# Kernel tuning notes

Measured on AMD Instinct MI355X. Metric: run time of the kernel, lower is better.

Reference implementation:

```python
import jax, jax.numpy as jnp
import numpy as np

B, L, D, N, NBLK = 16, 2048, 256, 64, 6  # 6 S4D layers: blocks 1,2,3,5 + 2 inner layers of FS4Ddeq


def setup_inputs() -> dict:
    key = jax.random.key(0)
    ks = jax.random.split(key, 12)
    x = jax.random.normal(ks[0], (B, L), dtype=jnp.float32)
    W_emb = jax.random.normal(ks[1], (1, D), dtype=jnp.float32) * 0.1
    b_emb = jnp.zeros((D,), jnp.float32)
    # S4D parameters, stacked over the 6 layers
    log_dt = jax.random.uniform(ks[2], (NBLK, D), minval=float(np.log(1e-3)), maxval=float(np.log(1e-1)), dtype=jnp.float32)
    logAre = jnp.full((NBLK, D, N), float(np.log(0.5)), jnp.float32)
    Aim = jnp.broadcast_to(jnp.pi * jnp.arange(N, dtype=jnp.float32), (NBLK, D, N)) * jnp.ones((NBLK, D, N), jnp.float32)
    Cre = jax.random.normal(ks[3], (NBLK, D, N), dtype=jnp.float32) * (0.5 ** 0.5)
    Cim = jax.random.normal(ks[4], (NBLK, D, N), dtype=jnp.float32) * (0.5 ** 0.5)
    Dskip = jax.random.normal(ks[5], (NBLK, D), dtype=jnp.float32)
    Wout = jax.random.normal(ks[6], (NBLK, D, D), dtype=jnp.float32) / np.sqrt(D)
    bout = jnp.zeros((NBLK, D), jnp.float32)
    gamma = jnp.ones((NBLK, D), jnp.float32)
    beta = jnp.zeros((NBLK, D), jnp.float32)
    # feedforward of the FS4Ddeq block (feed_size=[B,L,emb_dim], feed_act='relu')
    feed_W1 = jax.random.normal(ks[7], (D, D), dtype=jnp.float32) / np.sqrt(D)
    feed_b1 = jnp.zeros((D,), jnp.float32)
    feed_W2 = jax.random.normal(ks[8], (D, D), dtype=jnp.float32) / np.sqrt(D)
    feed_b2 = jnp.zeros((D,), jnp.float32)
    fc_W = jax.random.normal(ks[9], (D, 2), dtype=jnp.float32) / np.sqrt(D)
    fc_b = jnp.zeros((2,), jnp.float32)
    return dict(x=x, W_emb=W_emb, b_emb=b_emb, log_dt=log_dt, logAre=logAre, Aim=Aim,
                Cre=Cre, Cim=Cim, Dskip=Dskip, Wout=Wout, bout=bout, gamma=gamma, beta=beta,
                feed_W1=feed_W1, feed_b1=feed_b1, feed_W2=feed_W2, feed_b2=feed_b2,
                fc_W=fc_W, fc_b=fc_b)


def _s4d_block(h, log_dt, logAre, Aim, Cre, Cim, Dskip, Wout, bout, gamma, beta):
    """Pre-norm (BN eval-mode) -> diagonal SSM (ZOH, FFT conv) -> GELU -> Linear -> residual."""
    _, Lh, _ = h.shape
    z = gamma * h + beta  # BatchNorm in eval mode with identity running stats
    dt = jnp.exp(log_dt)[:, None]                      # [D,1]
    A = -jnp.exp(logAre) + 1j * Aim                    # [D,N] diagonal state matrix
    dtA = dt * A                                       # [D,N]
    C = (Cre + 1j * Cim) * (jnp.exp(dtA) - 1.0) / A    # ZOH-discretized C*B
    # Vandermonde kernel K[d,l] = 2*Re sum_n C[d,n] * exp(dtA[d,n])^l
    vand = jnp.exp(dtA[:, :, None] * jnp.arange(Lh, dtype=jnp.float32))  # [D,N,L]
    K = 2.0 * jnp.einsum('dn,dnl->dl', C, vand).real   # [D,L]
    u = jnp.transpose(z, (0, 2, 1))                    # [B,D,L]
    kf = jnp.fft.rfft(K, n=2 * Lh)
    uf = jnp.fft.rfft(u, n=2 * Lh)
    y = jnp.fft.irfft(uf * kf, n=2 * Lh)[..., :Lh]     # causal conv
    y = y + Dskip[:, None] * u                         # feedthrough D
    y = jax.nn.gelu(jnp.transpose(y, (0, 2, 1)))       # [B,L,D]
    y = jnp.einsum('bld,de->ble', y, Wout) + bout      # output projection
    return y + h                                       # skip connection


def reference(x, W_emb, b_emb, log_dt, logAre, Aim, Cre, Cim, Dskip, Wout, bout,
              gamma, beta, feed_W1, feed_b1, feed_W2, feed_b2, fc_W, fc_b):
    h = x[..., None] @ W_emb + b_emb  # nn.Linear(1, emb_dim): [B,L,D]
    # layers 1,2,3,5: S4D blocks (dropout is identity in eval mode)
    for i in range(4):
        h = _s4d_block(h, log_dt[i], logAre[i], Aim[i], Cre[i], Cim[i],
                       Dskip[i], Wout[i], bout[i], gamma[i], beta[i])
    # layer4: FS4Ddeq_model with layers=2 inner S4D blocks + relu feed net + final relu + skip
    r = h
    for i in (4, 5):
        h = _s4d_block(h, log_dt[i], logAre[i], Aim[i], Cre[i], Cim[i],
                       Dskip[i], Wout[i], bout[i], gamma[i], beta[i])
    h = jax.nn.relu(h @ feed_W1 + feed_b1) @ feed_W2 + feed_b2
    h = jax.nn.relu(h + r)
    mean_y = jnp.mean(h, axis=1)       # [B,D]
    logits = mean_y @ fc_W + fc_b      # [B,2]
    return logits
```

## Files before the change

### kernel.cpp

```cpp
#include <hip/hip_runtime.h>
#include <hip/hip_fp16.h>
#include <math.h>

#define B_ 16
#define L_ 2048
#define D_ 256
#define N_ 64
#define NBLK_ 6
#define LC_ 128
#define NC_ 16

typedef _Float16 half8 __attribute__((ext_vector_type(8)));
typedef float f32x4 __attribute__((ext_vector_type(4)));

__device__ __forceinline__ unsigned short f2h(float f) {
  _Float16 h = (_Float16)f;
  return *(unsigned short*)&h;
}
__device__ __forceinline__ float h2f(unsigned short u) {
  _Float16 h = *(_Float16*)&u;
  return (float)h;
}

__global__ void precompute_kernel(const float* __restrict__ log_dt,
                                  const float* __restrict__ logAre,
                                  const float* __restrict__ Aim,
                                  const float* __restrict__ Cre,
                                  const float* __restrict__ Cim,
                                  float* __restrict__ wbuf,
                                  float* __restrict__ c2buf,
                                  float* __restrict__ wlbuf) {
  int idx = blockIdx.x * blockDim.x + threadIdx.x;
  if (idx >= NBLK_ * D_ * N_) return;
  int blk = idx >> 14;
  int rem = idx & 16383;
  int d = rem >> 6;
  int n = rem & 63;
  float dt   = expf(log_dt[blk * D_ + d]);
  float are  = -expf(logAre[idx]);
  float aim  = Aim[idx];
  float dtar = dt * are, dtai = dt * aim;
  float er = expf(dtar);
  float wr = er * cosf(dtai);
  float wi = er * sinf(dtai);
  float inv = 1.0f / (are * are + aim * aim);
  float wm1r = wr - 1.0f;
  float br = (wm1r * are + wi * aim) * inv;
  float bi = (wi * are - wm1r * aim) * inv;
  float crv = Cre[idx], civ = Cim[idx];
  float c2r = 2.0f * (crv * br - civ * bi);
  float c2i = 2.0f * (crv * bi + civ * br);
  float eL = expf((float)LC_ * dtar);
  float angL = (float)LC_ * dtai;
  float* wb = wbuf + (size_t)((blk << 8) + d) * 128;
  wb[n] = wr; wb[64 + n] = wi;
  float* cb = c2buf + (size_t)((blk << 8) + d) * 128;
  cb[n] = c2r; cb[64 + n] = c2i;
  wlbuf[2 * idx] = eL * cosf(angL); wlbuf[2 * idx + 1] = eL * sinf(angL);
}

__global__ __launch_bounds__(256) void build_all(
    const float* __restrict__ WB, const float* __restrict__ C2B,
    const float* __restrict__ WLB,
    const float* __restrict__ gamma_, const float* __restrict__ beta_,
    const float* __restrict__ dskip,
    unsigned short* __restrict__ TnA, unsigned short* __restrict__ EnA,
    unsigned short* __restrict__ FnA, float* __restrict__ PbetaA,
    float* __restrict__ SbetaA) {
  __shared__ float Pr[128][65];
  __shared__ float Pi_[128][65];
  __shared__ float wc[256];
  __shared__ float Kt[128];
  int bid = blockIdx.x;
  int blk = bid >> 8, d = bid & 255;
  int t = threadIdx.x;
  if (t < 128) wc[t] = WB[(size_t)((blk << 8) + d) * 128 + t];
  else         wc[t] = C2B[(size_t)((blk << 8) + d) * 128 + (t - 128)];
  __syncthreads();
  int n = t & 63, tj = t >> 6;
  float wr = wc[n], wi = wc[64 + n];
  float gd = gamma_[blk * D_ + d], bd = beta_[blk * D_ + d], dsk = dskip[blk * D_ + d];
  {
    int j0 = tj << 5;
    float pr = 1.f, pi = 0.f, br = wr, bi = wi;
    int e = j0;
    while (e) {
      if (e & 1) { float tt = pr * br - pi * bi; pi = pr * bi + pi * br; pr = tt; }
      float t2 = br * br - bi * bi; bi = 2.f * br * bi; br = t2;
      e >>= 1;
    }
#pragma unroll 4
    for (int k = 0; k < 32; ++k) {
      Pr[j0 + k][n] = pr; Pi_[j0 + k][n] = pi;
      float tt = pr * wr - pi * wi; pi = pr * wi + pi * wr; pr = tt;
    }
  }
  __syncthreads();
  if (t < 128) {
    float kc = 0.f;
    for (int nn = 0; nn < 64; ++nn)
      kc += wc[128 + nn] * Pr[t][nn] - wc[192 + nn] * Pi_[t][nn];
    Kt[t] = kc + (t == 0 ? dsk : 0.f);
  }
  size_t mbase = (size_t)(blk * 256 + d) * 16384;
#pragma unroll
  for (int r8 = 0; r8 < 8; ++r8) {
    int task = t + (r8 << 8);
    int j = task >> 4, g = task & 15;
    int half = g >> 3, n0 = (g & 7) << 3;
    unsigned short v[8];
#pragma unroll
    for (int i = 0; i < 8; ++i) {
      int nn = n0 + i;
      float pr = Pr[j][nn], pi = Pi_[j][nn];
      float wwr = wc[nn], wwi = wc[64 + nn];
      float qr = pr * wwr - pi * wwi, qi = pr * wwi + pi * wwr;
      float cr = wc[128 + nn], ci = wc[192 + nn];
      v[i] = f2h(half == 0 ? (cr * qr - ci * qi) : (cr * qi + ci * qr));
    }
    *(uint4*)(EnA + mbase + (size_t)j * 128 + (half << 6) + n0) = *(uint4*)v;
  }
#pragma unroll
  for (int r8 = 0; r8 < 8; ++r8) {
    int task = t + (r8 << 8);
    int n2 = task >> 4, tb = task & 15;
    int half = n2 >> 6, nn = n2 & 63;
    int tau0 = tb << 3;
    unsigned short v[8];
#pragma unroll
    for (int i = 0; i < 8; ++i) {
      int j = 127 - (tau0 + i);
      v[i] = f2h(half == 0 ? (gd * Pr[j][nn]) : (-gd * Pi_[j][nn]));
    }
    *(uint4*)(FnA + mbase + (size_t)n2 * 128 + tau0) = *(uint4*)v;
  }
  __syncthreads();
  if (t < 128) {
    float ps = 0.f;
    for (int t2 = 0; t2 <= t; ++t2) ps += Kt[t2];
    PbetaA[((size_t)blk * 256 + d) * 128 + t] = bd * ps;
  }
  if (t >= 128 && t < 192) {
    int nn = t - 128;
    const float* wlp = WLB + (((size_t)((blk << 8) + d)) * 64 + nn) * 2;
    float wlr = wlp[0], wli = wlp[1];
    float wwr = wc[nn], wwi = wc[64 + nn];
    float nr = wlr - 1.f, ni = wli, dr2 = wwr - 1.f, di = wwi;
    float iv = 1.f / (dr2 * dr2 + di * di);
    SbetaA[((size_t)blk * 256 + d) * 128 + nn]      = bd * ((nr * dr2 + ni * di) * iv);
    SbetaA[((size_t)blk * 256 + d) * 128 + 64 + nn] = bd * (-((ni * dr2 - nr * di) * iv));
  }
  int chunk = t & 15, rg = t >> 4;
#pragma unroll
  for (int it = 0; it < 8; ++it) {
    int trow = (it << 4) + rg;
    int tau0 = chunk << 3;
    unsigned short v[8];
#pragma unroll
    for (int i = 0; i < 8; ++i) {
      int tau = tau0 + i;
      v[i] = (tau <= trow) ? f2h(gd * Kt[trow - tau]) : (unsigned short)0;
    }
    *(uint4*)(TnA + mbase + (size_t)trow * 128 + tau0) = *(uint4*)v;
  }
}

__global__ void embed_kernel(const float* __restrict__ x, const float* __restrict__ wemb,
                             const float* __restrict__ bemb, unsigned short* __restrict__ H) {
  int tid = blockIdx.x * blockDim.x + threadIdx.x;
  if (tid >= B_ * L_ * D_) return;
  int d = tid & (D_ - 1);
  int lg = tid >> 8;
  H[tid] = f2h(fmaf(x[lg], wemb[d], bemb[d]));
}

__global__ __launch_bounds__(256) void trans_h_ut(const unsigned short* __restrict__ H,
                                                  unsigned short* __restrict__ UT) {
  __shared__ __align__(16) unsigned short lds[64][136];
  int bi = blockIdx.x;
  int bc = bi >> 2, dq = bi & 3;
  int b = bc >> 4, ch = bc & 15;
  int tid = threadIdx.x;
  const unsigned short* src = H + ((size_t)(b * L_ + ch * 128)) * D_ + dq * 64;
  int tau0 = tid >> 4;
  int dl = (tid & 15) << 2;
  for (int tt = 0; tt < 128; tt += 16) {
    ushort4 v = *(const ushort4*)(src + (size_t)(tt + tau0) * D_ + dl);
    lds[dl + 0][tt + tau0] = v.x;
    lds[dl + 1][tt + tau0] = v.y;
    lds[dl + 2][tt + tau0] = v.z;
    lds[dl + 3][tt + tau0] = v.w;
  }
  __syncthreads();
  int r = tid >> 2, seg = (tid & 3) << 5;
  unsigned short* dst = UT + ((size_t)((dq * 64 + r) * 256 + bc)) * 128 + seg;
  const unsigned short* srow = &lds[r][seg];
  *(uint4*)(dst + 0)  = *(const uint4*)(srow + 0);
  *(uint4*)(dst + 8)  = *(const uint4*)(srow + 8);
  *(uint4*)(dst + 16) = *(const uint4*)(srow + 16);
  *(uint4*)(dst + 24) = *(const uint4*)(srow + 24);
}

__global__ __launch_bounds__(256) void scan_fused(
    const unsigned short* __restrict__ UT, const unsigned short* __restrict__ FnA,
    const unsigned short* __restrict__ TnA, const unsigned short* __restrict__ EnA,
    const float* __restrict__ SbetaA, const float* __restrict__ PbetaA,
    const float* __restrict__ WLB, unsigned short* __restrict__ GT, int blk) {
  __shared__ __align__(16) unsigned short SLl[256 * 136];
  __shared__ __align__(16) unsigned short AsB[128 * 40];
  __shared__ __align__(16) unsigned short BsB[128 * 40];
  _Float16* As = (_Float16*)AsB;
  _Float16* Bs = (_Float16*)BsB;
  int d = blockIdx.x;
  int tid = threadIdx.x, lane = tid & 63, w = tid >> 6;
  int wm = (w & 1) << 6, wn = (w >> 1) << 6;
  int r = tid & 127, sg = (tid >> 7) << 4;
  int cn = lane & 15, rq = lane >> 4;
  int ko = (lane >> 4) << 3;
  const unsigned short* Au = UT + (size_t)d * 256 * 128;
  const unsigned short* Bf = FnA + (size_t)(blk * 256 + d) * 16384;
  const unsigned short* Bt = TnA + (size_t)(blk * 256 + d) * 16384;
  const unsigned short* Be = EnA + (size_t)(blk * 256 + d) * 16384;
  size_t pb = ((size_t)blk * 256 + d) * 128;

  for (int mh = 0; mh < 2; ++mh) {
    const unsigned short* Ab = Au + (size_t)(mh << 7) * 128;
    f32x4 acc[4][4];
#pragma unroll
    for (int a = 0; a < 4; ++a)
#pragma unroll
      for (int b2 = 0; b2 < 4; ++b2) acc[a][b2] = (f32x4){0.f, 0.f, 0.f, 0.f};
    uint4 a0 = *(const uint4*)(Ab + (size_t)r * 128 + sg);
    uint4 a1 = *(const uint4*)(Ab + (size_t)r * 128 + sg + 8);
    uint4 b0 = *(const uint4*)(Bf + (size_t)r * 128 + sg);
    uint4 b1 = *(const uint4*)(Bf + (size_t)r * 128 + sg + 8);
    for (int kc = 0; kc < 128; kc += 32) {
      __syncthreads();
      *(uint4*)&As[r * 40 + sg] = a0; *(uint4*)&As[r * 40 + sg + 8] = a1;
      *(uint4*)&Bs[r * 40 + sg] = b0; *(uint4*)&Bs[r * 40 + sg + 8] = b1;
      __syncthreads();
      if (kc < 96) {
        a0 = *(const uint4*)(Ab + (size_t)r * 128 + kc + 32 + sg);
        a1 = *(const uint4*)(Ab + (size_t)r * 128 + kc + 32 + sg + 8);
        b0 = *(const uint4*)(Bf + (size_t)r * 128 + kc + 32 + sg);
        b1 = *(const uint4*)(Bf + (size_t)r * 128 + kc + 32 + sg + 8);
      }
      half8 af[4], bf4[4];
#pragma unroll
      for (int mf = 0; mf < 4; ++mf) af[mf] = *(const half8*)&As[(wm + (mf << 4) + cn) * 40 + ko];
#pragma unroll
      for (int nf = 0; nf < 4; ++nf) bf4[nf] = *(const half8*)&Bs[(wn + (nf << 4) + cn) * 40 + ko];
#pragma unroll
      for (int mf = 0; mf < 4; ++mf)
#pragma unroll
        for (int nf = 0; nf < 4; ++nf)
          acc[mf][nf] = __builtin_amdgcn_mfma_f32_16x16x32_f16(af[mf], bf4[nf], acc[mf][nf], 0, 0, 0);
    }
#pragma unroll
    for (int nf = 0; nf < 4; ++nf) {
      int nl = wn + (nf << 4) + cn;
      float sb = SbetaA[pb + nl];
#pragma unroll
      for (int mf = 0; mf < 4; ++mf)
#pragma unroll
        for (int rr = 0; rr < 4; ++rr) {
          int row = (mh << 7) + wm + (mf << 4) + (rq << 2) + rr;
          SLl[row * 136 + nl] = f2h(acc[mf][nf][rr] + sb);
        }
    }
  }
  __syncthreads();

  for (int task = tid; task < 1024; task += 256) {
    int b = task >> 6, n = task & 63;
    const float* wlp = WLB + (((size_t)((blk << 8) + d)) * 64 + n) * 2;
    float wlr = wlp[0], wli = wlp[1];
    float Sr = 0.f, Sj = 0.f;
    for (int c = 0; c < NC_; ++c) {
      int row = (b << 4) + c;
      float tr2 = h2f(SLl[row * 136 + n]);
      float tj  = h2f(SLl[row * 136 + 64 + n]);
      SLl[row * 136 + n]      = f2h(Sr);
      SLl[row * 136 + 64 + n] = f2h(Sj);
      float nSr = fmaf(wlr, Sr, fmaf(wli, Sj, tr2));
      Sj = fmaf(-wli, Sr, fmaf(wlr, Sj, tj));
      Sr = nSr;
    }
  }
  __syncthreads();

  for (int mh = 0; mh < 2; ++mh) {
    const unsigned short* Ab = Au + (size_t)(mh << 7) * 128;
    const _Float16* SA = (const _Float16*)SLl + (size_t)(mh << 7) * 136;
    f32x4 acc[4][4];
#pragma unroll
    for (int a = 0; a < 4; ++a)
#pragma unroll
      for (int b2 = 0; b2 < 4; ++b2) acc[a][b2] = (f32x4){0.f, 0.f, 0.f, 0.f};
    uint4 a0 = *(const uint4*)(Ab + (size_t)r * 128 + sg);
    uint4 a1 = *(const uint4*)(Ab + (size_t)r * 128 + sg + 8);
    uint4 b0 = *(const uint4*)(Bt + (size_t)r * 128 + sg);
    uint4 b1 = *(const uint4*)(Bt + (size_t)r * 128 + sg + 8);
    for (int kb = 0; kb < 8; ++kb) {
      __syncthreads();
      if (kb < 4) { *(uint4*)&As[r * 40 + sg] = a0; *(uint4*)&As[r * 40 + sg + 8] = a1; }
      *(uint4*)&Bs[r * 40 + sg] = b0; *(uint4*)&Bs[r * 40 + sg + 8] = b1;
      __syncthreads();
      if (kb < 3) {
        int kc = (kb + 1) << 5;
        a0 = *(const uint4*)(Ab + (size_t)r * 128 + kc + sg);
        a1 = *(const uint4*)(Ab + (size_t)r * 128 + kc + sg + 8);
        b0 = *(const uint4*)(Bt + (size_t)r * 128 + kc + sg);
        b1 = *(const uint4*)(Bt + (size_t)r * 128 + kc + sg + 8);
      } else if (kb < 7) {
        int kc = (kb - 3) << 5;
        b0 = *(const uint4*)(Be + (size_t)r * 128 + kc + sg);
        b1 = *(const uint4*)(Be + (size_t)r * 128 + kc + sg + 8);
      }
      half8 af[4], bf4[4];
      if (kb < 4) {
#pragma unroll
        for (int mf = 0; mf < 4; ++mf) af[mf] = *(const half8*)&As[(wm + (mf << 4) + cn) * 40 + ko];
      } else {
        int kof = ((kb - 4) << 5) + ko;
#pragma unroll
        for (int mf = 0; mf < 4; ++mf) af[mf] = *(const half8*)&SA[(wm + (mf << 4) + cn) * 136 + kof];
      }
#pragma unroll
      for (int nf = 0; nf < 4; ++nf) bf4[nf] = *(const half8*)&Bs[(wn + (nf << 4) + cn) * 40 + ko];
#pragma unroll
      for (int mf = 0; mf < 4; ++mf)
#pragma unroll
        for (int nf = 0; nf < 4; ++nf)
          acc[mf][nf] = __builtin_amdgcn_mfma_f32_16x16x32_f16(af[mf], bf4[nf], acc[mf][nf], 0, 0, 0);
    }
    __syncthreads();
    unsigned short* epi = SLl + (size_t)(mh << 7) * 136;
#pragma unroll
    for (int nf = 0; nf < 4; ++nf) {
      int nl = wn + (nf << 4) + cn;
      float pb2 = PbetaA[pb + nl];
#pragma unroll
      for (int mf = 0; mf < 4; ++mf)
#pragma unroll
        for (int rr = 0; rr < 4; ++rr) {
          int ml = wm + (mf << 4) + (rq << 2) + rr;
          float xx = acc[mf][nf][rr] + pb2;
          float x3 = xx * xx * xx;
          float inner = 0.7978845608028654f * fmaf(0.044715f, x3, xx);
          float e = __expf(-2.f * fabsf(inner));
          float th = (1.f - e) / (1.f + e);
          th = copysignf(th, inner);
          epi[ml * 136 + nl] = f2h(0.5f * xx * (1.f + th));
        }
    }
    __syncthreads();
    int mr = tid >> 1, hf = (tid & 1) << 6;
    size_t gb = ((size_t)d * 256 + (mh << 7) + mr) * 128 + hf;
#pragma unroll
    for (int k = 0; k < 8; ++k)
      *(uint4*)(GT + gb + k * 8) = *(const uint4*)&epi[mr * 136 + hf + k * 8];
  }
}

__global__ void wprep_kernel(const float* __restrict__ Wout, const float* __restrict__ fW1,
                             const float* __restrict__ fW2, unsigned short* __restrict__ WT) {
  __shared__ float tile[64][65];
  int wv = blockIdx.x >> 4;
  int tk = (blockIdx.x >> 2) & 3;
  int tn = blockIdx.x & 3;
  const float* src = (wv < 6) ? (Wout + (size_t)wv * 65536) : (wv == 6 ? fW1 : fW2);
  int r = threadIdx.x >> 4;
  int c = (threadIdx.x & 15) << 2;
  for (int rr = 0; rr < 64; rr += 16) {
    float4 v = *(const float4*)(src + (size_t)(tk * 64 + r + rr) * 256 + tn * 64 + c);
    tile[r + rr][c] = v.x; tile[r + rr][c + 1] = v.y;
    tile[r + rr][c + 2] = v.z; tile[r + rr][c + 3] = v.w;
  }
  __syncthreads();
  for (int rr = 0; rr < 64; rr += 16) {
    int n = r + rr;
    ushort4 o;
    o.x = f2h(tile[c + 0][n]); o.y = f2h(tile[c + 1][n]);
    o.z = f2h(tile[c + 2][n]); o.w = f2h(tile[c + 3][n]);
    *(ushort4*)(WT + (size_t)wv * 65536 + (size_t)(tn * 64 + n) * 256 + tk * 64 + c) = o;
  }
}

__global__ __launch_bounds__(256, 2) void gemm_gt(const unsigned short* __restrict__ GT,
    const unsigned short* __restrict__ Wt, const float* __restrict__ bias,
    const unsigned short* __restrict__ res, unsigned short* __restrict__ hout,
    unsigned short* __restrict__ ut_next) {
  __shared__ __align__(16) unsigned short smem[18432];
  unsigned short* As = smem;
  unsigned short* Bs = smem + 9216;
  int tid = threadIdx.x;
  int bid = blockIdx.x;
  int bc = bid & 255;
  int m0 = bc * 128, n0 = (bid >> 8) << 7;
  int lane = tid & 63, w = tid >> 6;
  int wm = (w & 1) << 6, wn = (w >> 1) << 6;
  int rb = tid >> 3, cb = (tid & 7) << 3;
  int dr = tid >> 2, sg = (tid & 3) << 5;
  f32x4 acc[4][4];
#pragma unroll
  for (int mf = 0; mf < 4; ++mf)
#pragma unroll
    for (int nf = 0; nf < 4; ++nf) acc[mf][nf] = (f32x4){0.f, 0.f, 0.f, 0.f};

  uint4 gv[4], bv[4];
  {
    const uint4* grow = (const uint4*)(GT + ((size_t)(dr * 256 + bc)) * 128 + sg);
    gv[0] = grow[0]; gv[1] = grow[1]; gv[2] = grow[2]; gv[3] = grow[3];
#pragma unroll
    for (int rr = 0; rr < 4; ++rr)
      bv[rr] = *(const uint4*)(Wt + (size_t)(n0 + rb + rr * 32) * 256 + cb);
  }
  for (int kb = 0; kb < 4; ++kb) {
    __syncthreads();
    const unsigned short* pv = (const unsigned short*)gv;
#pragma unroll
    for (int i = 0; i < 32; ++i) As[(sg + i) * 72 + dr] = pv[i];
#pragma unroll
    for (int rr = 0; rr < 4; ++rr) *(uint4*)&Bs[(rb + rr * 32) * 72 + cb] = bv[rr];
    __syncthreads();
    if (kb < 3) {
      int k0 = (kb + 1) << 6;
      const uint4* grow = (const uint4*)(GT + ((size_t)((k0 + dr) * 256 + bc)) * 128 + sg);
      gv[0] = grow[0]; gv[1] = grow[1]; gv[2] = grow[2]; gv[3] = grow[3];
#pragma unroll
      for (int rr = 0; rr < 4; ++rr)
        bv[rr] = *(const uint4*)(Wt + (size_t)(n0 + rb + rr * 32) * 256 + k0 + cb);
    }
#pragma unroll
    for (int kw = 0; kw < 2; ++kw) {
      int ko = (kw << 5) + ((lane >> 4) << 3);
      half8 af[4], bfr[4];
#pragma unroll
      for (int mf = 0; mf < 4; ++mf)
        af[mf] = *(const half8*)&As[(wm + (mf << 4) + (lane & 15)) * 72 + ko];
#pragma unroll
      for (int nf = 0; nf < 4; ++nf)
        bfr[nf] = *(const half8*)&Bs[(wn + (nf << 4) + (lane & 15)) * 72 + ko];
#pragma unroll
      for (int mf = 0; mf < 4; ++mf)
#pragma unroll
        for (int nf = 0; nf < 4; ++nf)
          acc[mf][nf] = __builtin_amdgcn_mfma_f32_16x16x32_f16(af[mf], bfr[nf], acc[mf][nf], 0, 0, 0);
    }
  }
  int cn = lane & 15, rq = lane >> 4;
  __syncthreads();
  unsigned short* epi = smem;
#pragma unroll
  for (int nf = 0; nf < 4; ++nf) {
    int nl = wn + (nf << 4) + cn;
    float bv2 = bias[n0 + nl];
#pragma unroll
    for (int mf = 0; mf < 4; ++mf)
#pragma unroll
      for (int r = 0; r < 4; ++r) {
        int ml = wm + (mf << 4) + (rq << 2) + r;
        float v = acc[mf][nf][r] + bv2 + h2f(res[(size_t)(m0 + ml) * 256 + n0 + nl]);
        epi[ml * 136 + nl] = f2h(v);
      }
  }
  __syncthreads();
  {
    int mr = tid >> 1, hf = (tid & 1) << 6;
    unsigned short* dst = hout + (size_t)(m0 + mr) * 256 + n0 + hf;
    const unsigned short* srow = epi + mr * 136 + hf;
#pragma unroll
    for (int k = 0; k < 8; ++k) *(uint4*)(dst + k * 8) = *(const uint4*)(srow + k * 8);
  }
  if (ut_next) {
    int nl = tid >> 1, h2 = (tid & 1) << 6;
    unsigned short* dst = ut_next + ((size_t)(n0 + nl) * 256 + bc) * 128 + h2;
#pragma unroll
    for (int k = 0; k < 8; ++k) {
      unsigned short v8[8];
#pragma unroll
      for (int e = 0; e < 8; ++e) v8[e] = epi[(h2 + k * 8 + e) * 136 + nl];
      *(uint4*)(dst + k * 8) = *(uint4*)v8;
    }
  }
}

__global__ __launch_bounds__(256, 2) void gemm_ffn(const unsigned short* __restrict__ A,
    const unsigned short* __restrict__ Wt, const float* __restrict__ bias,
    const unsigned short* __restrict__ res, unsigned short* __restrict__ outp) {
  __shared__ __align__(16) unsigned short smem[18432];
  unsigned short* As = smem;
  unsigned short* Bs = smem + 9216;
  int tid = threadIdx.x;
  int bid = blockIdx.x;
  int m0 = (bid & 255) << 7, n0 = (bid >> 8) << 7;
  int lane = tid & 63, w = tid >> 6;
  int wm = (w & 1) << 6, wn = (w >> 1) << 6;
  int r0 = tid >> 3;
  int c0 = (tid & 7) << 3;
  f32x4 acc[4][4];
#pragma unroll
  for (int mf = 0; mf < 4; ++mf)
#pragma unroll
    for (int nf = 0; nf < 4; ++nf) acc[mf][nf] = (f32x4){0.f, 0.f, 0.f, 0.f};

  uint4 av[4], bv[4];
#pragma unroll
  for (int rr = 0; rr < 4; ++rr) {
    int r = r0 + rr * 32;
    av[rr] = *(const uint4*)(A + (size_t)(m0 + r) * 256 + c0);
    bv[rr] = *(const uint4*)(Wt + (size_t)(n0 + r) * 256 + c0);
  }
  for (int kb = 0; kb < 4; ++kb) {
    __syncthreads();
#pragma unroll
    for (int rr = 0; rr < 4; ++rr) {
      int r = r0 + rr * 32;
      *(uint4*)&As[r * 72 + c0] = av[rr];
      *(uint4*)&Bs[r * 72 + c0] = bv[rr];
    }
    __syncthreads();
    if (kb < 3) {
      int k0 = (kb + 1) << 6;
#pragma unroll
      for (int rr = 0; rr < 4; ++rr) {
        int r = r0 + rr * 32;
        av[rr] = *(const uint4*)(A + (size_t)(m0 + r) * 256 + k0 + c0);
        bv[rr] = *(const uint4*)(Wt + (size_t)(n0 + r) * 256 + k0 + c0);
      }
    }
#pragma unroll
    for (int kw = 0; kw < 2; ++kw) {
      int ko = (kw << 5) + ((lane >> 4) << 3);
      half8 af[4], bfr[4];
#pragma unroll
      for (int mf = 0; mf < 4; ++mf)
        af[mf] = *(const half8*)&As[(wm + (mf << 4) + (lane & 15)) * 72 + ko];
#pragma unroll
      for (int nf = 0; nf < 4; ++nf)
        bfr[nf] = *(const half8*)&Bs[(wn + (nf << 4) + (lane & 15)) * 72 + ko];
#pragma unroll
      for (int mf = 0; mf < 4; ++mf)
#pragma unroll
        for (int nf = 0; nf < 4; ++nf)
          acc[mf][nf] = __builtin_amdgcn_mfma_f32_16x16x32_f16(af[mf], bfr[nf], acc[mf][nf], 0, 0, 0);
    }
  }
  int cn = lane & 15, rq = lane >> 4;
  __syncthreads();
  unsigned short* epi = smem;
#pragma unroll
  for (int nf = 0; nf < 4; ++nf) {
    int nl = wn + (nf << 4) + cn;
#pragma unroll
    for (int mf = 0; mf < 4; ++mf)
#pragma unroll
      for (int r = 0; r < 4; ++r) {
        int ml = wm + (mf << 4) + (rq << 2) + r;
        epi[ml * 136 + nl] = f2h(acc[mf][nf][r]);
      }
  }
  __syncthreads();
  int mr = tid >> 1, hf = (tid & 1) << 6;
  unsigned short* dst = outp + (size_t)(m0 + mr) * 256 + n0 + hf;
#pragma unroll
  for (int k = 0; k < 8; ++k) {
    uint4 c = *(const uint4*)&epi[mr * 136 + hf + k * 8];
    uint4 rv = (uint4){0, 0, 0, 0};
    if (res) rv = *(const uint4*)(res + (size_t)(m0 + mr) * 256 + n0 + hf + k * 8);
    const unsigned short* cp = (const unsigned short*)&c;
    const unsigned short* rp = (const unsigned short*)&rv;
    unsigned short o8[8];
#pragma unroll
    for (int e = 0; e < 8; ++e) {
      float v = h2f(cp[e]) + bias[n0 + hf + k * 8 + e];
      if (res) v += h2f(rp[e]);
      o8[e] = f2h(fmaxf(v, 0.f));
    }
    *(uint4*)(dst + k * 8) = *(uint4*)o8;
  }
}

__global__ void head1_kernel(const unsigned short* __restrict__ H, float* __restrict__ part) {
  int b = blockIdx.x, ls = blockIdx.y, d = threadIdx.x;
  const unsigned short* p = H + ((size_t)(b * L_ + ls * 128)) * D_ + d;
  float sum = 0.f;
  for (int l = 0; l < 128; ++l) sum += h2f(p[(size_t)l * D_]);
  part[(b * 16 + ls) * D_ + d] = sum;
}

__global__ void head2_kernel(const float* __restrict__ part, const float* __restrict__ fcW,
                             const float* __restrict__ fcb, float* __restrict__ out) {
  int b = blockIdx.x, d = threadIdx.x;
  float sum = 0.f;
  for (int i = 0; i < 16; ++i) sum += part[(b * 16 + i) * D_ + d];
  __shared__ float meanv[D_];
  meanv[d] = sum * (1.0f / (float)L_);
  __syncthreads();
  if (d < 2) {
    float accv = fcb[d];
    for (int k = 0; k < D_; ++k) accv = fmaf(meanv[k], fcW[k * 2 + d], accv);
    out[b * 2 + d] = accv;
  }
}

extern "C" void kernel_launch(void* const* d_in, const int* in_sizes, int n_in,
                              void* d_out, int out_size, void* d_ws, size_t ws_size,
                              hipStream_t stream) {
  const float* x      = (const float*)d_in[0];
  const float* W_emb  = (const float*)d_in[1];
  const float* b_emb  = (const float*)d_in[2];
  const float* log_dt = (const float*)d_in[3];
  const float* logAre = (const float*)d_in[4];
  const float* Aim    = (const float*)d_in[5];
  const float* Cre    = (const float*)d_in[6];
  const float* Cim    = (const float*)d_in[7];
  const float* Dskip  = (const float*)d_in[8];
  const float* Wout   = (const float*)d_in[9];
  const float* bout   = (const float*)d_in[10];
  const float* gamma_ = (const float*)d_in[11];
  const float* beta_  = (const float*)d_in[12];
  const float* fW1    = (const float*)d_in[13];
  const float* fb1    = (const float*)d_in[14];
  const float* fW2    = (const float*)d_in[15];
  const float* fb2    = (const float*)d_in[16];
  const float* fcW    = (const float*)d_in[17];
  const float* fcb    = (const float*)d_in[18];
  float* outp = (float*)d_out;

  const size_t HSZ = (size_t)B_ * L_ * D_;
  float* WB     = (float*)d_ws;
  float* C2B    = WB + (size_t)NBLK_ * D_ * 128;
  float* WLB    = C2B + (size_t)NBLK_ * D_ * 128;
  float* PbetaA = WLB + (size_t)NBLK_ * D_ * N_ * 2;
  float* SbetaA = PbetaA + (size_t)NBLK_ * 32768;
  unsigned short* H   = (unsigned short*)(SbetaA + (size_t)NBLK_ * 32768);
  unsigned short* R   = H + HSZ;
  unsigned short* UT  = R + HSZ;
  unsigned short* GT  = UT + HSZ;
  unsigned short* Gbf = GT;
  unsigned short* TnA = GT + HSZ;
  unsigned short* EnA = TnA + (size_t)NBLK_ * 4194304;
  unsigned short* FnA = EnA + (size_t)NBLK_ * 4194304;
  unsigned short* WT  = FnA + (size_t)NBLK_ * 4194304;

  precompute_kernel<<<(NBLK_ * D_ * N_ + 255) / 256, 256, 0, stream>>>(
      log_dt, logAre, Aim, Cre, Cim, WB, C2B, WLB);
  wprep_kernel<<<128, 256, 0, stream>>>(Wout, fW1, fW2, WT);
  build_all<<<NBLK_ * 256, 256, 0, stream>>>(WB, C2B, WLB, gamma_, beta_, Dskip,
                                             TnA, EnA, FnA, PbetaA, SbetaA);
  embed_kernel<<<(B_ * L_ * D_ + 255) / 256, 256, 0, stream>>>(x, W_emb, b_emb, H);
  trans_h_ut<<<1024, 256, 0, stream>>>(H, UT);

  const unsigned short* hin_t[6]  = {H, H, H, H, R, H};
  unsigned short*       hout_t[6] = {H, H, H, R, H, H};
  for (int i = 0; i < 6; ++i) {
    scan_fused<<<256, 256, 0, stream>>>(UT, FnA, TnA, EnA, SbetaA, PbetaA, WLB, GT, i);
    gemm_gt<<<512, 256, 0, stream>>>(
        GT, WT + (size_t)i * 65536, bout + i * D_, hin_t[i], hout_t[i],
        (i < 5) ? UT : nullptr);
  }
  gemm_ffn<<<512, 256, 0, stream>>>(H, WT + (size_t)6 * 65536, fb1, nullptr, Gbf);
  gemm_ffn<<<512, 256, 0, stream>>>(Gbf, WT + (size_t)7 * 65536, fb2, R, H);
  head1_kernel<<<dim3(16, 16), 256, 0, stream>>>(H, WB);
  head2_kernel<<<16, 256, 0, stream>>>(WB, fcW, fcb, outp);
}
```

Before: 633.6 us.

## Fuse SSM matrix construction into scan kernel, build operands in LDS

Removes the separate build_all kernel that wrote the per-channel Fn/Tn/En fp16 matrices (about 150 MB total) to global memory. scan_fused now generates these operands directly in LDS (Bm1/Bm2) for each block and channel, computing Kt with a wave shuffle reduction, and computes Sbeta/Pbeta in shared memory. This removes a large global write and read stream, at the cost of extra on-chip compute per scan launch and much higher LDS usage per block, which may lower occupancy. The gemm epilogue loop order is also swapped.

Result: faster. 610.5 us (-3.6%).

```diff
diff --git a/kernel.cpp b/kernel.cpp
--- a/kernel.cpp
+++ b/kernel.cpp
@@ -59,112 +59,6 @@
   wlbuf[2 * idx] = eL * cosf(angL); wlbuf[2 * idx + 1] = eL * sinf(angL);
 }
 
-__global__ __launch_bounds__(256) void build_all(
-    const float* __restrict__ WB, const float* __restrict__ C2B,
-    const float* __restrict__ WLB,
-    const float* __restrict__ gamma_, const float* __restrict__ beta_,
-    const float* __restrict__ dskip,
-    unsigned short* __restrict__ TnA, unsigned short* __restrict__ EnA,
-    unsigned short* __restrict__ FnA, float* __restrict__ PbetaA,
-    float* __restrict__ SbetaA) {
-  __shared__ float Pr[128][65];
-  __shared__ float Pi_[128][65];
-  __shared__ float wc[256];
-  __shared__ float Kt[128];
-  int bid = blockIdx.x;
-  int blk = bid >> 8, d = bid & 255;
-  int t = threadIdx.x;
-  if (t < 128) wc[t] = WB[(size_t)((blk << 8) + d) * 128 + t];
-  else         wc[t] = C2B[(size_t)((blk << 8) + d) * 128 + (t - 128)];
-  __syncthreads();
-  int n = t & 63, tj = t >> 6;
-  float wr = wc[n], wi = wc[64 + n];
-  float gd = gamma_[blk * D_ + d], bd = beta_[blk * D_ + d], dsk = dskip[blk * D_ + d];
-  {
-    int j0 = tj << 5;
-    float pr = 1.f, pi = 0.f, br = wr, bi = wi;
-    int e = j0;
-    while (e) {
-      if (e & 1) { float tt = pr * br - pi * bi; pi = pr * bi + pi * br; pr = tt; }
-      float t2 = br * br - bi * bi; bi = 2.f * br * bi; br = t2;
-      e >>= 1;
-    }
-#pragma unroll 4
-    for (int k = 0; k < 32; ++k) {
-      Pr[j0 + k][n] = pr; Pi_[j0 + k][n] = pi;
-      float tt = pr * wr - pi * wi; pi = pr * wi + pi * wr; pr = tt;
-    }
-  }
-  __syncthreads();
-  if (t < 128) {
-    float kc = 0.f;
-    for (int nn = 0; nn < 64; ++nn)
-      kc += wc[128 + nn] * Pr[t][nn] - wc[192 + nn] * Pi_[t][nn];
-    Kt[t] = kc + (t == 0 ? dsk : 0.f);
-  }
-  size_t mbase = (size_t)(blk * 256 + d) * 16384;
-#pragma unroll
-  for (int r8 = 0; r8 < 8; ++r8) {
-    int task = t + (r8 << 8);
-    int j = task >> 4, g = task & 15;
-    int half = g >> 3, n0 = (g & 7) << 3;
-    unsigned short v[8];
-#pragma unroll
-    for (int i = 0; i < 8; ++i) {
-      int nn = n0 + i;
-      float pr = Pr[j][nn], pi = Pi_[j][nn];
-      float wwr = wc[nn], wwi = wc[64 + nn];
-      float qr = pr * wwr - pi * wwi, qi = pr * wwi + pi * wwr;
-      float cr = wc[128 + nn], ci = wc[192 + nn];
-      v[i] = f2h(half == 0 ? (cr * qr - ci * qi) : (cr * qi + ci * qr));
-    }
-    *(uint4*)(EnA + mbase + (size_t)j * 128 + (half << 6) + n0) = *(uint4*)v;
-  }
-#pragma unroll
-  for (int r8 = 0; r8 < 8; ++r8) {
-    int task = t + (r8 << 8);
-    int n2 = task >> 4, tb = task & 15;
-    int half = n2 >> 6, nn = n2 & 63;
-    int tau0 = tb << 3;
-    unsigned short v[8];
-#pragma unroll
-    for (int i = 0; i < 8; ++i) {
-      int j = 127 - (tau0 + i);
-      v[i] = f2h(half == 0 ? (gd * Pr[j][nn]) : (-gd * Pi_[j][nn]));
-    }
-    *(uint4*)(FnA + mbase + (size_t)n2 * 128 + tau0) = *(uint4*)v;
-  }
-  __syncthreads();
-  if (t < 128) {
-    float ps = 0.f;
-    for (int t2 = 0; t2 <= t; ++t2) ps += Kt[t2];
-    PbetaA[((size_t)blk * 256 + d) * 128 + t] = bd * ps;
-  }
-  if (t >= 128 && t < 192) {
-    int nn = t - 128;
-    const float* wlp = WLB + (((size_t)((blk << 8) + d)) * 64 + nn) * 2;
-    float wlr = wlp[0], wli = wlp[1];
-    float wwr = wc[nn], wwi = wc[64 + nn];
-    float nr = wlr - 1.f, ni = wli, dr2 = wwr - 1.f, di = wwi;
-    float iv = 1.f / (dr2 * dr2 + di * di);
-    SbetaA[((size_t)blk * 256 + d) * 128 + nn]      = bd * ((nr * dr2 + ni * di) * iv);
-    SbetaA[((size_t)blk * 256 + d) * 128 + 64 + nn] = bd * (-((ni * dr2 - nr * di) * iv));
-  }
-  int chunk = t & 15, rg = t >> 4;
-#pragma unroll
-  for (int it = 0; it < 8; ++it) {
-    int trow = (it << 4) + rg;
-    int tau0 = chunk << 3;
-    unsigned short v[8];
-#pragma unroll
-    for (int i = 0; i < 8; ++i) {
-      int tau = tau0 + i;
-      v[i] = (tau <= trow) ? f2h(gd * Kt[trow - tau]) : (unsigned short)0;
-    }
-    *(uint4*)(TnA + mbase + (size_t)trow * 128 + tau0) = *(uint4*)v;
-  }
-}
-
 __global__ void embed_kernel(const float* __restrict__ x, const float* __restrict__ wemb,
                              const float* __restrict__ bemb, unsigned short* __restrict__ H) {
   int tid = blockIdx.x * blockDim.x + threadIdx.x;
@@ -202,15 +96,21 @@
 }
 
 __global__ __launch_bounds__(256) void scan_fused(
-    const unsigned short* __restrict__ UT, const unsigned short* __restrict__ FnA,
-    const unsigned short* __restrict__ TnA, const unsigned short* __restrict__ EnA,
-    const float* __restrict__ SbetaA, const float* __restrict__ PbetaA,
-    const float* __restrict__ WLB, unsigned short* __restrict__ GT, int blk) {
+    const unsigned short* __restrict__ UT,
+    const float* __restrict__ WB, const float* __restrict__ C2B,
+    const float* __restrict__ WLB,
+    const float* __restrict__ gamma_, const float* __restrict__ beta_,
+    const float* __restrict__ dskip,
+    unsigned short* __restrict__ GT, int blk) {
   __shared__ __align__(16) unsigned short SLl[256 * 136];
+  __shared__ __align__(16) unsigned short Bm1[128 * 136];
+  __shared__ __align__(16) unsigned short Bm2[128 * 136];
   __shared__ __align__(16) unsigned short AsB[128 * 40];
-  __shared__ __align__(16) unsigned short BsB[128 * 40];
+  __shared__ float wc[256];
+  __shared__ float Kt[128];
+  __shared__ float Pb[128];
+  __shared__ float Sb[128];
   _Float16* As = (_Float16*)AsB;
-  _Float16* Bs = (_Float16*)BsB;
   int d = blockIdx.x;
   int tid = threadIdx.x, lane = tid & 63, w = tid >> 6;
   int wm = (w & 1) << 6, wn = (w >> 1) << 6;
@@ -218,10 +118,52 @@
   int cn = lane & 15, rq = lane >> 4;
   int ko = (lane >> 4) << 3;
   const unsigned short* Au = UT + (size_t)d * 256 * 128;
-  const unsigned short* Bf = FnA + (size_t)(blk * 256 + d) * 16384;
-  const unsigned short* Bt = TnA + (size_t)(blk * 256 + d) * 16384;
-  const unsigned short* Be = EnA + (size_t)(blk * 256 + d) * 16384;
-  size_t pb = ((size_t)blk * 256 + d) * 128;
+
+  if (tid < 128) wc[tid] = WB[(size_t)((blk << 8) + d) * 128 + tid];
+  else           wc[tid] = C2B[(size_t)((blk << 8) + d) * 128 + (tid - 128)];
+  __syncthreads();
+  int n = tid & 63, tj = tid >> 6;
+  float gd = gamma_[blk * D_ + d], bd = beta_[blk * D_ + d], dsk = dskip[blk * D_ + d];
+  {
+    float wr = wc[n], wi = wc[64 + n];
+    float c2r = wc[128 + n], c2i = wc[192 + n];
+    int j0 = tj << 5;
+    float pr = 1.f, pi = 0.f, br = wr, bi = wi;
+    int e = j0;
+    while (e) {
+      if (e & 1) { float tt = pr * br - pi * bi; pi = pr * bi + pi * br; pr = tt; }
+      float t2 = br * br - bi * bi; bi = 2.f * br * bi; br = t2;
+      e >>= 1;
+    }
+    for (int k2 = 0; k2 < 32; ++k2) {
+      int j = j0 + k2;
+      Bm1[n * 136 + (127 - j)]        = f2h(gd * pr);
+      Bm1[(64 + n) * 136 + (127 - j)] = f2h(-gd * pi);
+      float qr = pr * wr - pi * wi, qi = pr * wi + pi * wr;
+      Bm2[j * 136 + n]      = f2h(c2r * qr - c2i * qi);
+      Bm2[j * 136 + 64 + n] = f2h(c2r * qi + c2i * qr);
+      float kc = c2r * pr - c2i * pi;
+#pragma unroll
+      for (int off = 1; off < 64; off <<= 1) kc += __shfl_xor(kc, off);
+      if (n == 0) Kt[j] = kc + (j == 0 ? dsk : 0.f);
+      pr = qr; pi = qi;
+    }
+  }
+  if (tid < 64) {
+    const float* wlp = WLB + (((size_t)((blk << 8) + d)) * 64 + tid) * 2;
+    float wlr = wlp[0], wli = wlp[1];
+    float nr = wlr - 1.f, ni = wli;
+    float dr2 = wc[tid] - 1.f, di = wc[64 + tid];
+    float iv = 1.f / (dr2 * dr2 + di * di);
+    Sb[tid]      = bd * ((nr * dr2 + ni * di) * iv);
+    Sb[64 + tid] = bd * (-((ni * dr2 - nr * di) * iv));
+  }
+  __syncthreads();
+  if (tid < 128) {
+    float ps = 0.f;
+    for (int t2 = 0; t2 <= tid; ++t2) ps += Kt[t2];
+    Pb[tid] = bd * ps;
+  }
 
   for (int mh = 0; mh < 2; ++mh) {
     const unsigned short* Ab = Au + (size_t)(mh << 7) * 128;
@@ -232,24 +174,20 @@
       for (int b2 = 0; b2 < 4; ++b2) acc[a][b2] = (f32x4){0.f, 0.f, 0.f, 0.f};
     uint4 a0 = *(const uint4*)(Ab + (size_t)r * 128 + sg);
     uint4 a1 = *(const uint4*)(Ab + (size_t)r * 128 + sg + 8);
-    uint4 b0 = *(const uint4*)(Bf + (size_t)r * 128 + sg);
-    uint4 b1 = *(const uint4*)(Bf + (size_t)r * 128 + sg + 8);
     for (int kc = 0; kc < 128; kc += 32) {
       __syncthreads();
       *(uint4*)&As[r * 40 + sg] = a0; *(uint4*)&As[r * 40 + sg + 8] = a1;
-      *(uint4*)&Bs[r * 40 + sg] = b0; *(uint4*)&Bs[r * 40 + sg + 8] = b1;
       __syncthreads();
       if (kc < 96) {
         a0 = *(const uint4*)(Ab + (size_t)r * 128 + kc + 32 + sg);
         a1 = *(const uint4*)(Ab + (size_t)r * 128 + kc + 32 + sg + 8);
-        b0 = *(const uint4*)(Bf + (size_t)r * 128 + kc + 32 + sg);
-        b1 = *(const uint4*)(Bf + (size_t)r * 128 + kc + 32 + sg + 8);
       }
       half8 af[4], bf4[4];
 #pragma unroll
       for (int mf = 0; mf < 4; ++mf) af[mf] = *(const half8*)&As[(wm + (mf << 4) + cn) * 40 + ko];
 #pragma unroll
-      for (int nf = 0; nf < 4; ++nf) bf4[nf] = *(const half8*)&Bs[(wn + (nf << 4) + cn) * 40 + ko];
+      for (int nf = 0; nf < 4; ++nf)
+        bf4[nf] = *(const half8*)((const _Float16*)Bm1 + (wn + (nf << 4) + cn) * 136 + kc + ko);
 #pragma unroll
       for (int mf = 0; mf < 4; ++mf)
 #pragma unroll
@@ -259,7 +197,7 @@
 #pragma unroll
     for (int nf = 0; nf < 4; ++nf) {
       int nl = wn + (nf << 4) + cn;
-      float sb = SbetaA[pb + nl];
+      float sb = Sb[nl];
 #pragma unroll
       for (int mf = 0; mf < 4; ++mf)
 #pragma unroll
@@ -272,19 +210,36 @@
   __syncthreads();
 
   for (int task = tid; task < 1024; task += 256) {
-    int b = task >> 6, n = task & 63;
-    const float* wlp = WLB + (((size_t)((blk << 8) + d)) * 64 + n) * 2;
+    int b = task >> 6, nn = task & 63;
+    const float* wlp = WLB + (((size_t)((blk << 8) + d)) * 64 + nn) * 2;
     float wlr = wlp[0], wli = wlp[1];
     float Sr = 0.f, Sj = 0.f;
     for (int c = 0; c < NC_; ++c) {
       int row = (b << 4) + c;
-      float tr2 = h2f(SLl[row * 136 + n]);
-      float tj  = h2f(SLl[row * 136 + 64 + n]);
-      SLl[row * 136 + n]      = f2h(Sr);
-      SLl[row * 136 + 64 + n] = f2h(Sj);
+      float tr2 = h2f(SLl[row * 136 + nn]);
+      float tj2 = h2f(SLl[row * 136 + 64 + nn]);
+      SLl[row * 136 + nn]      = f2h(Sr);
+      SLl[row * 136 + 64 + nn] = f2h(Sj);
       float nSr = fmaf(wlr, Sr, fmaf(wli, Sj, tr2));
-      Sj = fmaf(-wli, Sr, fmaf(wlr, Sj, tj));
+      Sj = fmaf(-wli, Sr, fmaf(wlr, Sj, tj2));
       Sr = nSr;
+    }
+  }
+  __syncthreads();
+
+  {
+    int chunk = tid & 15, rg = tid >> 4;
+#pragma unroll
+    for (int it = 0; it < 8; ++it) {
+      int trow = (it << 4) + rg;
+      int tau0 = chunk << 3;
+      unsigned short v[8];
+#pragma unroll
+      for (int i = 0; i < 8; ++i) {
+        int tau = tau0 + i;
+        v[i] = (tau <= trow) ? f2h(gd * Kt[trow - tau]) : (unsigned short)0;
+      }
+      *(uint4*)(Bm1 + (size_t)trow * 136 + tau0) = *(uint4*)v;
     }
   }
   __syncthreads();
@@ -299,35 +254,31 @@
       for (int b2 = 0; b2 < 4; ++b2) acc[a][b2] = (f32x4){0.f, 0.f, 0.f, 0.f};
     uint4 a0 = *(const uint4*)(Ab + (size_t)r * 128 + sg);
     uint4 a1 = *(const uint4*)(Ab + (size_t)r * 128 + sg + 8);
-    uint4 b0 = *(const uint4*)(Bt + (size_t)r * 128 + sg);
-    uint4 b1 = *(const uint4*)(Bt + (size_t)r * 128 + sg + 8);
     for (int kb = 0; kb < 8; ++kb) {
-      __syncthreads();
-      if (kb < 4) { *(uint4*)&As[r * 40 + sg] = a0; *(uint4*)&As[r * 40 + sg + 8] = a1; }
-      *(uint4*)&Bs[r * 40 + sg] = b0; *(uint4*)&Bs[r * 40 + sg + 8] = b1;
-      __syncthreads();
-      if (kb < 3) {
-        int kc = (kb + 1) << 5;
-        a0 = *(const uint4*)(Ab + (size_t)r * 128 + kc + sg);
-        a1 = *(const uint4*)(Ab + (size_t)r * 128 + kc + sg + 8);
-        b0 = *(const uint4*)(Bt + (size_t)r * 128 + kc + sg);
-        b1 = *(const uint4*)(Bt + (size_t)r * 128 + kc + sg + 8);
-      } else if (kb < 7) {
-        int kc = (kb - 3) << 5;
-        b0 = *(const uint4*)(Be + (size_t)r * 128 + kc + sg);
-        b1 = *(const uint4*)(Be + (size_t)r * 128 + kc + sg + 8);
-      }
+      int kc = (kb & 3) << 5;
       half8 af[4], bf4[4];
       if (kb < 4) {
+        __syncthreads();
+        *(uint4*)&As[r * 40 + sg] = a0; *(uint4*)&As[r * 40 + sg + 8] = a1;
+        __syncthreads();
+        if (kb < 3) {
+          int kc2 = (kb + 1) << 5;
+          a0 = *(const uint4*)(Ab + (size_t)r * 128 + kc2 + sg);
+          a1 = *(const uint4*)(Ab + (size_t)r * 128 + kc2 + sg + 8);
+        }
 #pragma unroll
         for (int mf = 0; mf < 4; ++mf) af[mf] = *(const half8*)&As[(wm + (mf << 4) + cn) * 40 + ko];
+#pragma unroll
+        for (int nf = 0; nf < 4; ++nf)
+          bf4[nf] = *(const half8*)((const _Float16*)Bm1 + (wn + (nf << 4) + cn) * 136 + kc + ko);
       } else {
-        int kof = ((kb - 4) << 5) + ko;
-#pragma unroll
-        for (int mf = 0; mf < 4; ++mf) af[mf] = *(const half8*)&SA[(wm + (mf << 4) + cn) * 136 + kof];
+#pragma unroll
+        for (int mf = 0; mf < 4; ++mf)
+          af[mf] = *(const half8*)&SA[(wm + (mf << 4) + cn) * 136 + kc + ko];
+#pragma unroll
+        for (int nf = 0; nf < 4; ++nf)
+          bf4[nf] = *(const half8*)((const _Float16*)Bm2 + (wn + (nf << 4) + cn) * 136 + kc + ko);
       }
-#pragma unroll
-      for (int nf = 0; nf < 4; ++nf) bf4[nf] = *(const half8*)&Bs[(wn + (nf << 4) + cn) * 40 + ko];
 #pragma unroll
       for (int mf = 0; mf < 4; ++mf)
 #pragma unroll
@@ -339,7 +290,7 @@
 #pragma unroll
     for (int nf = 0; nf < 4; ++nf) {
       int nl = wn + (nf << 4) + cn;
-      float pb2 = PbetaA[pb + nl];
+      float pb2 = Pb[nl];
 #pragma unroll
       for (int mf = 0; mf < 4; ++mf)
 #pragma unroll
@@ -554,12 +505,13 @@
   for (int nf = 0; nf < 4; ++nf) {
     int nl = wn + (nf << 4) + cn;
 #pragma unroll
-    for (int mf = 0; mf < 4; ++mf)
-#pragma unroll
-      for (int r = 0; r < 4; ++r) {
+    for (int r = 0; r < 4; ++r) {
+#pragma unroll
+      for (int mf = 0; mf < 4; ++mf) {
         int ml = wm + (mf << 4) + (rq << 2) + r;
         epi[ml * 136 + nl] = f2h(acc[mf][nf][r]);
       }
+    }
   }
   __syncthreads();
   int mr = tid >> 1, hf = (tid & 1) << 6;
@@ -633,30 +585,23 @@
   float* WB     = (float*)d_ws;
   float* C2B    = WB + (size_t)NBLK_ * D_ * 128;
   float* WLB    = C2B + (size_t)NBLK_ * D_ * 128;
-  float* PbetaA = WLB + (size_t)NBLK_ * D_ * N_ * 2;
-  float* SbetaA = PbetaA + (size_t)NBLK_ * 32768;
-  unsigned short* H   = (unsigned short*)(SbetaA + (size_t)NBLK_ * 32768);
+  unsigned short* H   = (unsigned short*)(WLB + (size_t)NBLK_ * D_ * N_ * 2);
   unsigned short* R   = H + HSZ;
   unsigned short* UT  = R + HSZ;
   unsigned short* GT  = UT + HSZ;
   unsigned short* Gbf = GT;
-  unsigned short* TnA = GT + HSZ;
-  unsigned short* EnA = TnA + (size_t)NBLK_ * 4194304;
-  unsigned short* FnA = EnA + (size_t)NBLK_ * 4194304;
-  unsigned short* WT  = FnA + (size_t)NBLK_ * 4194304;
+  unsigned short* WT  = GT + HSZ;
 
   precompute_kernel<<<(NBLK_ * D_ * N_ + 255) / 256, 256, 0, stream>>>(
       log_dt, logAre, Aim, Cre, Cim, WB, C2B, WLB);
   wprep_kernel<<<128, 256, 0, stream>>>(Wout, fW1, fW2, WT);
-  build_all<<<NBLK_ * 256, 256, 0, stream>>>(WB, C2B, WLB, gamma_, beta_, Dskip,
-                                             TnA, EnA, FnA, PbetaA, SbetaA);
   embed_kernel<<<(B_ * L_ * D_ + 255) / 256, 256, 0, stream>>>(x, W_emb, b_emb, H);
   trans_h_ut<<<1024, 256, 0, stream>>>(H, UT);
 
   const unsigned short* hin_t[6]  = {H, H, H, H, R, H};
   unsigned short*       hout_t[6] = {H, H, H, R, H, H};
   for (int i = 0; i < 6; ++i) {
-    scan_fused<<<256, 256, 0, stream>>>(UT, FnA, TnA, EnA, SbetaA, PbetaA, WLB, GT, i);
+    scan_fused<<<256, 256, 0, stream>>>(UT, WB, C2B, WLB, gamma_, beta_, Dskip, GT, i);
     gemm_gt<<<512, 256, 0, stream>>>(
         GT, WT + (size_t)i * 65536, bout + i * D_, hin_t[i], hout_t[i],
         (i < 5) ? UT : nullptr);
```
